# Performance work log

Hardware: AMD Instinct MI355X
Metric: run time of the kernel (lower is better)

The kernel has to match this reference:

```python
import jax, jax.numpy as jnp
import numpy as np

N_NODES = 100000
N_EDGES = 1600000
N_EMBED = 48
N_CONVS = 6
N_GRAPHS = 1000
VOCAB = 100


def setup_inputs() -> dict:
    key = jax.random.key(0)
    ks = jax.random.split(key, 20)
    AtomicNum = jax.random.randint(ks[0], (N_NODES,), 0, VOCAB)
    Edge = jax.random.randint(ks[1], (2, N_EDGES), 0, N_NODES)
    graph_id = jnp.sort(jax.random.randint(ks[2], (N_NODES,), 0, N_GRAPHS))
    s = 1.0 / np.sqrt(N_EMBED)
    def lin(k):
        k1, k2 = jax.random.split(k)
        w = jax.random.uniform(k1, (N_EMBED, N_EMBED), jnp.float32, -s, s)
        b = jax.random.uniform(k2, (N_EMBED,), jnp.float32, -s, s)
        return w, b
    def stacked(k):
        ws, bs = zip(*[lin(kk) for kk in jax.random.split(k, N_CONVS)])
        return jnp.stack(ws), jnp.stack(bs)
    emb = jax.random.normal(ks[3], (VOCAB, N_EMBED), jnp.float32)
    msg_w1, msg_b1 = stacked(ks[4])
    msg_w2, msg_b2 = stacked(ks[5])
    upd_w1, upd_b1 = stacked(ks[6])
    upd_w2, upd_b2 = stacked(ks[7])
    ro_w1, ro_b1 = lin(ks[8])
    k1, k2 = jax.random.split(ks[9])
    ro_w2 = jax.random.uniform(k1, (N_EMBED, 1), jnp.float32, -s, s)
    ro_b2 = jax.random.uniform(k2, (1,), jnp.float32, -s, s)
    return dict(AtomicNum=AtomicNum, Edge=Edge, graph_id=graph_id, emb=emb,
                msg_w1=msg_w1, msg_b1=msg_b1, msg_w2=msg_w2, msg_b2=msg_b2,
                upd_w1=upd_w1, upd_b1=upd_b1, upd_w2=upd_w2, upd_b2=upd_b2,
                ro_w1=ro_w1, ro_b1=ro_b1, ro_w2=ro_w2, ro_b2=ro_b2)


def reference(AtomicNum, Edge, graph_id, emb,
              msg_w1, msg_b1, msg_w2, msg_b2,
              upd_w1, upd_b1, upd_w2, upd_b2,
              ro_w1, ro_b1, ro_w2, ro_b2):
    n_nodes = AtomicNum.shape[0]
    src, dst = Edge[0], Edge[1]
    h = emb[AtomicNum]  # [N, d]
    for l in range(N_CONVS):
        # gather endpoint features, elementwise product, message MLP
        x = h[src] * h[dst]                                      # [E, d]
        m = jax.nn.relu(x @ msg_w1[l] + msg_b1[l]) @ msg_w2[l] + msg_b2[l]
        agg = jax.ops.segment_sum(m, dst, num_segments=n_nodes)  # scatter_add
        u = jax.nn.relu(agg @ upd_w1[l] + upd_b1[l]) @ upd_w2[l] + upd_b2[l]
        h = h + u  # residual update
    y = jax.nn.relu(h @ ro_w1 + ro_b1) @ ro_w2 + ro_b2           # [N, 1]
    # per-graph sum readout (== torch.split by Natom + sum per chunk)
    out = jax.ops.segment_sum(y[:, 0], graph_id, num_segments=N_GRAPHS)
    return out
```

## Files before the change

kernel.cpp:

```cpp
#include <hip/hip_runtime.h>
#include <hip/hip_bf16.h>


#define NE 48
#define NB_SH 8

typedef __attribute__((ext_vector_type(8))) short short8;
typedef __attribute__((ext_vector_type(4))) float floatx4;

__device__ __forceinline__ unsigned short bf16_rne(float v) {
    unsigned u = __float_as_uint(v);
    u += 0x7FFFu + ((u >> 16) & 1u);
    return (unsigned short)(u >> 16);
}

__device__ __forceinline__ void split8p(const float* __restrict__ x, short8& hi, short8& lo) {
    union { unsigned u[4]; short8 s; } H, L;
#pragma unroll
    for (int i = 0; i < 4; ++i) {
        float a = x[2 * i], b = x[2 * i + 1];
        __hip_bfloat162 h2 = __float22bfloat162_rn(make_float2(a, b));
        unsigned h = *reinterpret_cast<unsigned*>(&h2);
        float ra = a - __uint_as_float(h << 16);
        float rb = b - __uint_as_float(h & 0xFFFF0000u);
        __hip_bfloat162 l2 = __float22bfloat162_rn(make_float2(ra, rb));
        H.u[i] = h;
        L.u[i] = *reinterpret_cast<unsigned*>(&l2);
    }
    hi = H.s; lo = L.s;
}

__device__ __forceinline__ void gemm3(const short8& ah0, const short8& al0,
                                      const short8& ah1, const short8& al1,
                                      const short8* __restrict__ hi,
                                      const short8* __restrict__ lo,
                                      int lane, floatx4* acc) {
#pragma unroll
    for (int t = 0; t < 3; ++t) {
        short8 bh0 = hi[(t * 2 + 0) * 64 + lane];
        short8 bh1 = hi[(t * 2 + 1) * 64 + lane];
        short8 bl0 = lo[(t * 2 + 0) * 64 + lane];
        short8 bl1 = lo[(t * 2 + 1) * 64 + lane];
        floatx4 c = {0.0f, 0.0f, 0.0f, 0.0f};
        c = __builtin_amdgcn_mfma_f32_16x16x32_bf16(ah0, bh0, c, 0, 0, 0);
        c = __builtin_amdgcn_mfma_f32_16x16x32_bf16(ah1, bh1, c, 0, 0, 0);
        c = __builtin_amdgcn_mfma_f32_16x16x32_bf16(al0, bh0, c, 0, 0, 0);
        c = __builtin_amdgcn_mfma_f32_16x16x32_bf16(al1, bh1, c, 0, 0, 0);
        c = __builtin_amdgcn_mfma_f32_16x16x32_bf16(ah0, bl0, c, 0, 0, 0);
        c = __builtin_amdgcn_mfma_f32_16x16x32_bf16(ah1, bl1, c, 0, 0, 0);
        acc[t] = c;
    }
}

__global__ __launch_bounds__(256) void embed_kernel(const int* __restrict__ an,
                                                    const float* __restrict__ emb,
                                                    float* __restrict__ h, int n4) {
    int i = blockIdx.x * 256 + threadIdx.x;
    if (i >= n4) return;
    int n = i / 12, q = i - n * 12;
    ((float4*)h)[i] = ((const float4*)emb)[an[n] * 12 + q];
}

__global__ __launch_bounds__(256) void hist_kernel(const int* __restrict__ dst,
                                                   int* __restrict__ cnt, int E) {
    int e = blockIdx.x * 256 + threadIdx.x;
    if (e < E) atomicAdd(&cnt[dst[e]], 1);
}

__global__ __launch_bounds__(256) void scansum_kernel(const int* __restrict__ cnt,
                                                      int* __restrict__ bsum, int N) {
    __shared__ int sw[4];
    const int tid = threadIdx.x, lane = tid & 63, wid = tid >> 6;
    int base = blockIdx.x * 1024;
    int v = 0;
#pragma unroll
    for (int k = 0; k < 4; ++k) {
        int i = base + k * 256 + tid;
        v += (i < N) ? cnt[i] : 0;
    }
#pragma unroll
    for (int o = 1; o < 64; o <<= 1) v += __shfl_xor(v, o, 64);
    if (lane == 0) sw[wid] = v;
    __syncthreads();
    if (tid == 0) bsum[blockIdx.x] = sw[0] + sw[1] + sw[2] + sw[3];
}

__global__ __launch_bounds__(256) void scanb_kernel(int* __restrict__ bsum, int nblk) {
    __shared__ int s[256];
    int tid = threadIdx.x;
    s[tid] = (tid < nblk) ? bsum[tid] : 0;
    __syncthreads();
    if (tid == 0) {
        int run = 0;
        for (int i = 0; i < nblk; ++i) { int t = s[i]; s[i] = run; run += t; }
    }
    __syncthreads();
    if (tid < nblk) bsum[tid] = s[tid];
}

__global__ __launch_bounds__(1024) void scanfix_kernel(const int* __restrict__ cnt,
                                                       const int* __restrict__ bsum,
                                                       int* __restrict__ offs,
                                                       int* __restrict__ gpos, int N) {
    __shared__ int swave[16];
    const int tid = threadIdx.x, lane = tid & 63, wid = tid >> 6;
    int i = blockIdx.x * 1024 + tid;
    int orig = (i < N) ? cnt[i] : 0;
    int v = orig;
#pragma unroll
    for (int off = 1; off < 64; off <<= 1) {
        int u = __shfl_up(v, off, 64);
        if (lane >= off) v += u;
    }
    if (lane == 63) swave[wid] = v;
    __syncthreads();
    if (wid == 0) {
        int w = (lane < 16) ? swave[lane] : 0;
#pragma unroll
        for (int off = 1; off < 16; off <<= 1) {
            int u = __shfl_up(w, off, 64);
            if (lane >= off) w += u;
        }
        if (lane < 16) swave[lane] = w;
    }
    __syncthreads();
    int prefix = (wid > 0) ? swave[wid - 1] : 0;
    int val = bsum[blockIdx.x] + prefix + v - orig;
    if (i < N) {
        offs[i] = val;
        if ((i & 255) == 0) gpos[i >> 8] = val;
    }
}

__global__ __launch_bounds__(256) void partA_kernel(const int* __restrict__ src,
                                                    const int* __restrict__ dst,
                                                    int* __restrict__ gpos,
                                                    int2* __restrict__ pairbuf,
                                                    int E, int NB) {
    __shared__ int lhist[512];
    __shared__ int lbase[512];
    const int tid = threadIdx.x;
    for (int i = tid; i < NB; i += 256) lhist[i] = 0;
    __syncthreads();
    const int base = blockIdx.x * 2048;
    int ssrc[8], sdst[8], rnk[8];
#pragma unroll
    for (int k = 0; k < 8; ++k) {
        int e = base + k * 256 + tid;
        if (e < E) {
            ssrc[k] = src[e]; sdst[k] = dst[e];
            rnk[k] = atomicAdd(&lhist[sdst[k] >> NB_SH], 1);
        }
    }
    __syncthreads();
    for (int i = tid; i < NB; i += 256) {
        int c = lhist[i];
        lbase[i] = c ? atomicAdd(&gpos[i], c) : 0;
    }
    __syncthreads();
#pragma unroll
    for (int k = 0; k < 8; ++k) {
        int e = base + k * 256 + tid;
        if (e < E)
            pairbuf[lbase[sdst[k] >> NB_SH] + rnk[k]] = make_int2(ssrc[k], sdst[k]);
    }
}

__global__ __launch_bounds__(256) void partB_kernel(const int2* __restrict__ pairbuf,
                                                    int* __restrict__ offs,
                                                    int* __restrict__ colsrc, int E) {
    int e = blockIdx.x * 256 + threadIdx.x;
    if (e < E) {
        int2 p = pairbuf[e];
        int pos = atomicAdd(&offs[p.y], 1);
        colsrc[pos] = p.x;
    }
}

__global__ __launch_bounds__(256) void pack_all_kernel(const float* __restrict__ w0,
                                                       const float* __restrict__ w1m,
                                                       const float* __restrict__ w2m,
                                                       const float* __restrict__ w3m,
                                                       const float* __restrict__ w4m,
                                                       short8* __restrict__ hi,
                                                       short8* __restrict__ lo) {
    int idx = blockIdx.x * 256 + threadIdx.x;
    if (idx >= 4 * 2304 + 384) return;
    int slot = idx / 2304;
    int rem  = idx - slot * 2304;
    const float* w = (slot == 0) ? w0 : (slot == 1) ? w1m : (slot == 2) ? w2m
                   : (slot == 3) ? w3m : w4m;
    int lane = rem & 63;
    int s = (rem >> 6) & 1;
    int t = (rem >> 7) % 3;
    int l = (rem >> 7) / 3;
    short8 h8, l8;
#pragma unroll
    for (int i = 0; i < 8; ++i) {
        int k = s * 32 + (lane >> 4) * 8 + i;
        int j = t * 16 + (lane & 15);
        float v = (k < NE) ? w[l * NE * NE + k * NE + j] : 0.0f;
        unsigned short hh = bf16_rne(v);
        float hf = __uint_as_float((unsigned)hh << 16);
        unsigned short ll = bf16_rne(v - hf);
        h8[i] = (short)hh;
        l8[i] = (short)ll;
    }
    hi[idx] = h8;
    lo[idx] = l8;
}

__global__ __launch_bounds__(256, 2) void layer_kernel(
    const float* __restrict__ hin,
    const int* __restrict__ colsrc,
    const int* __restrict__ ends,
    const int* __restrict__ cnt,
    float* __restrict__ hout,
    const short8* __restrict__ bhi,
    const short8* __restrict__ blo,
    const float* __restrict__ b1,
    const short8* __restrict__ w2hi, const short8* __restrict__ w2lo, const float* __restrict__ b2,
    const short8* __restrict__ u1hi, const short8* __restrict__ u1lo, const float* __restrict__ ub1,
    const short8* __restrict__ u2hi, const short8* __restrict__ u2lo, const float* __restrict__ ub2,
    int N,
    int final_layer,
    const int* __restrict__ gid,
    const short8* __restrict__ rw1hi, const short8* __restrict__ rw1lo,
    const float* __restrict__ rb1, const float* __restrict__ rw2,
    const float* __restrict__ rb2, float* __restrict__ out)
{
    __shared__ float tile[4][16][52];
    const int tid  = threadIdx.x;
    const int lane = tid & 63;
    const int wid  = tid >> 6;
    const int n0   = blockIdx.x * 64 + wid * 16;
    if (n0 >= N) return;

    const int m  = lane & 15;
    const int kb = lane >> 4;
    float (*mytile)[52] = tile[wid];

    short8 bh[6], bl[6];
#pragma unroll
    for (int i = 0; i < 6; ++i) { bh[i] = bhi[i * 64 + lane]; bl[i] = blo[i * 64 + lane]; }
    const float bb0 = b1[m], bb1 = b1[16 + m], bb2 = b1[32 + m];

#pragma unroll 1
    for (int nn = 0; nn < 16; ++nn) {
        const int n = n0 + nn;
        const int deg = cnt[n];
        const int end = ends[n];
        const int beg = end - deg;

        const float* hd = hin + (size_t)n * NE;
        float4 d0a = ((const float4*)(hd + kb * 8))[0];
        float4 d0b = ((const float4*)(hd + kb * 8))[1];
        float4 d1a = make_float4(0, 0, 0, 0), d1b = d1a;
        if (kb < 2) {
            d1a = ((const float4*)(hd + 32 + kb * 8))[0];
            d1b = ((const float4*)(hd + 32 + kb * 8))[1];
        }

        float s0 = 0.0f, s1 = 0.0f, s2 = 0.0f;
        const int ntile = (deg + 15) >> 4;

        for (int it = 0; it < ntile; ++it) {
            const int rem = deg - it * 16;
            int eidx = beg + it * 16 + m;
            int srow = colsrc[(m < rem) ? eidx : beg];
            const float* hs = hin + (size_t)srow * NE + kb * 8;

            float x0[8], x1[8];
            {
                float4 a0 = ((const float4*)hs)[0];
                float4 a1 = ((const float4*)hs)[1];
                x0[0] = a0.x * d0a.x; x0[1] = a0.y * d0a.y; x0[2] = a0.z * d0a.z; x0[3] = a0.w * d0a.w;
                x0[4] = a1.x * d0b.x; x0[5] = a1.y * d0b.y; x0[6] = a1.z * d0b.z; x0[7] = a1.w * d0b.w;
            }
            if (kb < 2) {
                float4 a0 = ((const float4*)(hs + 32))[0];
                float4 a1 = ((const float4*)(hs + 32))[1];
                x1[0] = a0.x * d1a.x; x1[1] = a0.y * d1a.y; x1[2] = a0.z * d1a.z; x1[3] = a0.w * d1a.w;
                x1[4] = a1.x * d1b.x; x1[5] = a1.y * d1b.y; x1[6] = a1.z * d1b.z; x1[7] = a1.w * d1b.w;
            } else {
#pragma unroll
                for (int i = 0; i < 8; ++i) x1[i] = 0.0f;
            }

            short8 ah0, al0, ah1, al1;
            split8p(x0, ah0, al0);
            split8p(x1, ah1, al1);

#pragma unroll
            for (int t = 0; t < 3; ++t) {
                short8 bh0 = bh[t * 2 + 0], bh1 = bh[t * 2 + 1];
                short8 bl0 = bl[t * 2 + 0], bl1 = bl[t * 2 + 1];
                floatx4 c = {0.0f, 0.0f, 0.0f, 0.0f};
                c = __builtin_amdgcn_mfma_f32_16x16x32_bf16(ah0, bh0, c, 0, 0, 0);
                c = __builtin_amdgcn_mfma_f32_16x16x32_bf16(ah1, bh1, c, 0, 0, 0);
                c = __builtin_amdgcn_mfma_f32_16x16x32_bf16(al0, bh0, c, 0, 0, 0);
                c = __builtin_amdgcn_mfma_f32_16x16x32_bf16(al1, bh1, c, 0, 0, 0);
                c = __builtin_amdgcn_mfma_f32_16x16x32_bf16(ah0, bl0, c, 0, 0, 0);
                c = __builtin_amdgcn_mfma_f32_16x16x32_bf16(ah1, bl1, c, 0, 0, 0);
                const float bb = (t == 0) ? bb0 : (t == 1) ? bb1 : bb2;
                float ts = 0.0f;
#pragma unroll
                for (int r = 0; r < 4; ++r) {
                    float v = fmaxf(c[r] + bb, 0.0f);
                    v = (kb * 4 + r < rem) ? v : 0.0f;
                    ts += v;
                }
                if (t == 0) s0 += ts; else if (t == 1) s1 += ts; else s2 += ts;
            }
        }

        s0 += __shfl_xor(s0, 16, 64); s0 += __shfl_xor(s0, 32, 64);
        s1 += __shfl_xor(s1, 16, 64); s1 += __shfl_xor(s1, 32, 64);
        s2 += __shfl_xor(s2, 16, 64); s2 += __shfl_xor(s2, 32, 64);

        float t1v = __shfl(s1, lane & 15, 64);
        float t2v = __shfl(s2, lane & 15, 64);
        float val = (lane < 16) ? s0 : (lane < 32) ? t1v : t2v;
        if (lane < 48) mytile[nn][lane] = val;
    }
    asm volatile("s_waitcnt lgkmcnt(0)" ::: "memory");

    float c0[8], c1[8];
    {
        const float* row = &mytile[m][0];
        *(float4*)(c0)     = *(const float4*)(row + kb * 8);
        *(float4*)(c0 + 4) = *(const float4*)(row + kb * 8 + 4);
        if (kb < 2) {
            *(float4*)(c1)     = *(const float4*)(row + 32 + kb * 8);
            *(float4*)(c1 + 4) = *(const float4*)(row + 32 + kb * 8 + 4);
        } else {
#pragma unroll
            for (int i = 0; i < 8; ++i) c1[i] = 0.0f;
        }
    }
    asm volatile("s_waitcnt lgkmcnt(0)" ::: "memory");
    short8 ah0, al0, ah1, al1;
    split8p(c0, ah0, al0);
    split8p(c1, ah1, al1);

    floatx4 acc[3];
    gemm3(ah0, al0, ah1, al1, w2hi, w2lo, lane, acc);

    {
        float b2j[3];
#pragma unroll
        for (int t = 0; t < 3; ++t) b2j[t] = b2[t * 16 + m];
#pragma unroll
        for (int r = 0; r < 4; ++r) {
            float fd = (float)cnt[n0 + kb * 4 + r];
#pragma unroll
            for (int t = 0; t < 3; ++t) acc[t][r] = fmaf(fd, b2j[t], acc[t][r]);
        }
    }

#pragma unroll
    for (int t = 0; t < 3; ++t)
#pragma unroll
        for (int r = 0; r < 4; ++r)
            mytile[kb * 4 + r][t * 16 + m] = acc[t][r];
    asm volatile("s_waitcnt lgkmcnt(0)" ::: "memory");
    {
        const float* row = &mytile[m][0];
        *(float4*)(c0)     = *(const float4*)(row + kb * 8);
        *(float4*)(c0 + 4) = *(const float4*)(row + kb * 8 + 4);
        if (kb < 2) {
            *(float4*)(c1)     = *(const float4*)(row + 32 + kb * 8);
            *(float4*)(c1 + 4) = *(const float4*)(row + 32 + kb * 8 + 4);
        } else {
#pragma unroll
            for (int i = 0; i < 8; ++i) c1[i] = 0.0f;
        }
    }
    asm volatile("s_waitcnt lgkmcnt(0)" ::: "memory");
    split8p(c0, ah0, al0);
    split8p(c1, ah1, al1);
    gemm3(ah0, al0, ah1, al1, u1hi, u1lo, lane, acc);
    {
        float bj[3];
#pragma unroll
        for (int t = 0; t < 3; ++t) bj[t] = ub1[t * 16 + m];
#pragma unroll
        for (int t = 0; t < 3; ++t)
#pragma unroll
            for (int r = 0; r < 4; ++r)
                acc[t][r] = fmaxf(acc[t][r] + bj[t], 0.0f);
    }

#pragma unroll
    for (int t = 0; t < 3; ++t)
#pragma unroll
        for (int r = 0; r < 4; ++r)
            mytile[kb * 4 + r][t * 16 + m] = acc[t][r];
    asm volatile("s_waitcnt lgkmcnt(0)" ::: "memory");
    {
        const float* row = &mytile[m][0];
        *(float4*)(c0)     = *(const float4*)(row + kb * 8);
        *(float4*)(c0 + 4) = *(const float4*)(row + kb * 8 + 4);
        if (kb < 2) {
            *(float4*)(c1)     = *(const float4*)(row + 32 + kb * 8);
            *(float4*)(c1 + 4) = *(const float4*)(row + 32 + kb * 8 + 4);
        } else {
#pragma unroll
            for (int i = 0; i < 8; ++i) c1[i] = 0.0f;
        }
    }
    asm volatile("s_waitcnt lgkmcnt(0)" ::: "memory");
    split8p(c0, ah0, al0);
    split8p(c1, ah1, al1);
    gemm3(ah0, al0, ah1, al1, u2hi, u2lo, lane, acc);

    {
        float bj[3];
#pragma unroll
        for (int t = 0; t < 3; ++t) bj[t] = ub2[t * 16 + m];
#pragma unroll
        for (int r = 0; r < 4; ++r) {
            const size_t row = (size_t)(n0 + kb * 4 + r) * NE;
#pragma unroll
            for (int t = 0; t < 3; ++t)
                acc[t][r] += hin[row + t * 16 + m] + bj[t];
        }
    }

    if (!final_layer) {
#pragma unroll
        for (int r = 0; r < 4; ++r) {
            const size_t row = (size_t)(n0 + kb * 4 + r) * NE;
#pragma unroll
            for (int t = 0; t < 3; ++t)
                hout[row + t * 16 + m] = acc[t][r];
        }
        return;
    }

#pragma unroll
    for (int t = 0; t < 3; ++t)
#pragma unroll
        for (int r = 0; r < 4; ++r)
            mytile[kb * 4 + r][t * 16 + m] = acc[t][r];
    asm volatile("s_waitcnt lgkmcnt(0)" ::: "memory");
    {
        const float* row = &mytile[m][0];
        *(float4*)(c0)     = *(const float4*)(row + kb * 8);
        *(float4*)(c0 + 4) = *(const float4*)(row + kb * 8 + 4);
        if (kb < 2) {
            *(float4*)(c1)     = *(const float4*)(row + 32 + kb * 8);
            *(float4*)(c1 + 4) = *(const float4*)(row + 32 + kb * 8 + 4);
        } else {
#pragma unroll
            for (int i = 0; i < 8; ++i) c1[i] = 0.0f;
        }
    }
    split8p(c0, ah0, al0);
    split8p(c1, ah1, al1);
    gemm3(ah0, al0, ah1, al1, rw1hi, rw1lo, lane, acc);

    float p[4] = {0.0f, 0.0f, 0.0f, 0.0f};
    {
        float bj[3], wj[3];
#pragma unroll
        for (int t = 0; t < 3; ++t) { bj[t] = rb1[t * 16 + m]; wj[t] = rw2[t * 16 + m]; }
#pragma unroll
        for (int t = 0; t < 3; ++t)
#pragma unroll
            for (int r = 0; r < 4; ++r)
                p[r] = fmaf(fmaxf(acc[t][r] + bj[t], 0.0f), wj[t], p[r]);
    }
#pragma unroll
    for (int o = 1; o < 16; o <<= 1) {
#pragma unroll
        for (int r = 0; r < 4; ++r) p[r] += __shfl_xor(p[r], o, 16);
    }
    if (m == 0) {
        float b2v = rb2[0];
#pragma unroll
        for (int r = 0; r < 4; ++r) {
            int n = n0 + kb * 4 + r;
            atomicAdd(out + gid[n], p[r] + b2v);
        }
    }
}

extern "C" void kernel_launch(void* const* d_in, const int* in_sizes, int n_in,
                              void* d_out, int out_size, void* d_ws, size_t ws_size,
                              hipStream_t stream) {
    const int*   AtomicNum = (const int*)  d_in[0];
    const int*   Edge      = (const int*)  d_in[1];
    const int*   graph_id  = (const int*)  d_in[2];
    const float* emb       = (const float*)d_in[3];
    const float* msg_w1    = (const float*)d_in[4];
    const float* msg_b1    = (const float*)d_in[5];
    const float* msg_w2    = (const float*)d_in[6];
    const float* msg_b2    = (const float*)d_in[7];
    const float* upd_w1    = (const float*)d_in[8];
    const float* upd_b1    = (const float*)d_in[9];
    const float* upd_w2    = (const float*)d_in[10];
    const float* upd_b2    = (const float*)d_in[11];
    const float* ro_w1     = (const float*)d_in[12];
    const float* ro_b1     = (const float*)d_in[13];
    const float* ro_w2     = (const float*)d_in[14];
    const float* ro_b2     = (const float*)d_in[15];

    const int N = in_sizes[0];
    const int E = in_sizes[1] / 2;
    const int* src = Edge;
    const int* dst = Edge + E;
    const int NB = (N + 255) >> NB_SH;
    const int NBLK = (N + 1023) / 1024;

    float*  h    = (float*)d_ws;
    float*  h2   = h  + (size_t)N * NE;
    int*    cnt  = (int*)(h2 + (size_t)N * NE);
    int*    offs = cnt + N;
    int*    colsrc = offs + N;
    short8* whi  = (short8*)(colsrc + E);
    short8* wlo  = whi + (4 * 2304 + 384);
    int*    gpos = (int*)(wlo + (4 * 2304 + 384));
    int*    bsum = gpos + NB;
    int2*   pairbuf = (int2*)h2;

    hipMemsetAsync(d_out, 0, (size_t)out_size * sizeof(float), stream);
    hipMemsetAsync(cnt, 0, (size_t)N * sizeof(int), stream);

    int n4 = N * 12;
    embed_kernel<<<(n4 + 255) / 256, 256, 0, stream>>>(AtomicNum, emb, h, n4);

    hist_kernel<<<(E + 255) / 256, 256, 0, stream>>>(dst, cnt, E);
    scansum_kernel<<<NBLK, 256, 0, stream>>>(cnt, bsum, N);
    scanb_kernel<<<1, 256, 0, stream>>>(bsum, NBLK);
    scanfix_kernel<<<NBLK, 1024, 0, stream>>>(cnt, bsum, offs, gpos, N);
    partA_kernel<<<(E + 2047) / 2048, 256, 0, stream>>>(src, dst, gpos, pairbuf, E, NB);
    partB_kernel<<<(E + 255) / 256, 256, 0, stream>>>(pairbuf, offs, colsrc, E);

    pack_all_kernel<<<(4 * 2304 + 384 + 255) / 256, 256, 0, stream>>>(
        msg_w1, msg_w2, upd_w1, upd_w2, ro_w1, whi, wlo);

    const float* hin = h;
    float* hout = h2;
    for (int l = 0; l < 6; ++l) {
        layer_kernel<<<(N + 63) / 64, 256, 0, stream>>>(
            hin, colsrc, offs, cnt, hout,
            whi + 0 * 2304 + (size_t)l * 384, wlo + 0 * 2304 + (size_t)l * 384,
            msg_b1 + (size_t)l * NE,
            whi + 1 * 2304 + (size_t)l * 384, wlo + 1 * 2304 + (size_t)l * 384, msg_b2 + (size_t)l * NE,
            whi + 2 * 2304 + (size_t)l * 384, wlo + 2 * 2304 + (size_t)l * 384, upd_b1 + (size_t)l * NE,
            whi + 3 * 2304 + (size_t)l * 384, wlo + 3 * 2304 + (size_t)l * 384, upd_b2 + (size_t)l * NE,
            N,
            (l == 5) ? 1 : 0,
            graph_id,
            whi + 4 * 2304, wlo + 4 * 2304,
            ro_b1, ro_w2, ro_b2, (float*)d_out);
        const float* tmp = hin; hin = hout; hout = (float*)tmp;
    }
}
```

Baseline: 870.0 us.

## Software-pipeline edge gathers across nodes with flattened tile cursor and LDS-staged dst rows

Replaces the per-node nested edge loop with a flattened cursor over all 16-edge tiles of the wave's 16 nodes. The colsrc index load runs two tiles ahead and the source-row gather one tile ahead, using double-buffered registers, so gather latency overlaps with the MFMA compute and does not stall at node boundaries. The wave's 16 destination rows are staged in LDS once and reused for the products and the residual add. Degrees are loaded once per lane and broadcast with shuffles. This costs extra registers and LDS, which could reduce occupancy, and adds branchy cursor logic.

```diff
diff --git a/kernel.cpp b/kernel.cpp
--- a/kernel.cpp
+++ b/kernel.cpp
@@ -209,6 +209,8 @@
     hi[idx] = h8;
     lo[idx] = l8;
 }
+
+struct Cur { int nn; int e0; int rem; };
 
 __global__ __launch_bounds__(256, 2) void layer_kernel(
     const float* __restrict__ hin,
@@ -230,6 +232,7 @@
     const float* __restrict__ rb2, float* __restrict__ out)
 {
     __shared__ float tile[4][16][52];
+    __shared__ float hdls[4][16][48];
     const int tid  = threadIdx.x;
     const int lane = tid & 63;
     const int wid  = tid >> 6;
@@ -239,89 +242,149 @@
     const int m  = lane & 15;
     const int kb = lane >> 4;
     float (*mytile)[52] = tile[wid];
+    float (*myhd)[48]   = hdls[wid];
+
+    {
+        const float4* sp = (const float4*)(hin + (size_t)n0 * NE);
+        float4* dp = (float4*)myhd;
+#pragma unroll
+        for (int f = 0; f < 3; ++f) dp[lane + f * 64] = sp[lane + f * 64];
+    }
+    const int mydeg = cnt[n0 + m];
+    const int myend = ends[n0 + m];
 
     short8 bh[6], bl[6];
 #pragma unroll
     for (int i = 0; i < 6; ++i) { bh[i] = bhi[i * 64 + lane]; bl[i] = blo[i * 64 + lane]; }
     const float bb0 = b1[m], bb1 = b1[16 + m], bb2 = b1[32 + m];
 
-#pragma unroll 1
-    for (int nn = 0; nn < 16; ++nn) {
-        const int n = n0 + nn;
-        const int deg = cnt[n];
-        const int end = ends[n];
-        const int beg = end - deg;
-
-        const float* hd = hin + (size_t)n * NE;
-        float4 d0a = ((const float4*)(hd + kb * 8))[0];
-        float4 d0b = ((const float4*)(hd + kb * 8))[1];
-        float4 d1a = make_float4(0, 0, 0, 0), d1b = d1a;
-        if (kb < 2) {
-            d1a = ((const float4*)(hd + 32 + kb * 8))[0];
-            d1b = ((const float4*)(hd + 32 + kb * 8))[1];
-        }
-
-        float s0 = 0.0f, s1 = 0.0f, s2 = 0.0f;
-        const int ntile = (deg + 15) >> 4;
-
-        for (int it = 0; it < ntile; ++it) {
-            const int rem = deg - it * 16;
-            int eidx = beg + it * 16 + m;
-            int srow = colsrc[(m < rem) ? eidx : beg];
-            const float* hs = hin + (size_t)srow * NE + kb * 8;
-
-            float x0[8], x1[8];
-            {
-                float4 a0 = ((const float4*)hs)[0];
-                float4 a1 = ((const float4*)hs)[1];
-                x0[0] = a0.x * d0a.x; x0[1] = a0.y * d0a.y; x0[2] = a0.z * d0a.z; x0[3] = a0.w * d0a.w;
-                x0[4] = a1.x * d0b.x; x0[5] = a1.y * d0b.y; x0[6] = a1.z * d0b.z; x0[7] = a1.w * d0b.w;
-            }
-            if (kb < 2) {
-                float4 a0 = ((const float4*)(hs + 32))[0];
-                float4 a1 = ((const float4*)(hs + 32))[1];
-                x1[0] = a0.x * d1a.x; x1[1] = a0.y * d1a.y; x1[2] = a0.z * d1a.z; x1[3] = a0.w * d1a.w;
-                x1[4] = a1.x * d1b.x; x1[5] = a1.y * d1b.y; x1[6] = a1.z * d1b.z; x1[7] = a1.w * d1b.w;
-            } else {
-#pragma unroll
-                for (int i = 0; i < 8; ++i) x1[i] = 0.0f;
-            }
-
-            short8 ah0, al0, ah1, al1;
-            split8p(x0, ah0, al0);
-            split8p(x1, ah1, al1);
-
-#pragma unroll
-            for (int t = 0; t < 3; ++t) {
-                short8 bh0 = bh[t * 2 + 0], bh1 = bh[t * 2 + 1];
-                short8 bl0 = bl[t * 2 + 0], bl1 = bl[t * 2 + 1];
-                floatx4 c = {0.0f, 0.0f, 0.0f, 0.0f};
-                c = __builtin_amdgcn_mfma_f32_16x16x32_bf16(ah0, bh0, c, 0, 0, 0);
-                c = __builtin_amdgcn_mfma_f32_16x16x32_bf16(ah1, bh1, c, 0, 0, 0);
-                c = __builtin_amdgcn_mfma_f32_16x16x32_bf16(al0, bh0, c, 0, 0, 0);
-                c = __builtin_amdgcn_mfma_f32_16x16x32_bf16(al1, bh1, c, 0, 0, 0);
-                c = __builtin_amdgcn_mfma_f32_16x16x32_bf16(ah0, bl0, c, 0, 0, 0);
-                c = __builtin_amdgcn_mfma_f32_16x16x32_bf16(ah1, bl1, c, 0, 0, 0);
-                const float bb = (t == 0) ? bb0 : (t == 1) ? bb1 : bb2;
-                float ts = 0.0f;
-#pragma unroll
-                for (int r = 0; r < 4; ++r) {
-                    float v = fmaxf(c[r] + bb, 0.0f);
-                    v = (kb * 4 + r < rem) ? v : 0.0f;
-                    ts += v;
-                }
-                if (t == 0) s0 += ts; else if (t == 1) s1 += ts; else s2 += ts;
-            }
-        }
-
+    {
+        float4 z = make_float4(0, 0, 0, 0);
+        float4* zp = (float4*)&mytile[lane >> 2][(lane & 3) * 12];
+        zp[0] = z; zp[1] = z; zp[2] = z;
+    }
+    asm volatile("s_waitcnt lgkmcnt(0)" ::: "memory");
+
+    auto nextc = [&](Cur c) -> Cur {
+        c.e0 += 16; c.rem -= 16;
+        while (c.rem <= 0) {
+            ++c.nn;
+            if (c.nn >= 16) { c.nn = 16; c.e0 = 0; c.rem = 1; return c; }
+            int d = __shfl(mydeg, c.nn, 64);
+            int e = __shfl(myend, c.nn, 64);
+            c.e0 = e - d; c.rem = d;
+        }
+        return c;
+    };
+    auto load_idx = [&](const Cur& c) -> int {
+        int off = (m < c.rem) ? m : 0;
+        return colsrc[c.e0 + off];
+    };
+
+    int curnode = -1;
+    float s0 = 0.0f, s1 = 0.0f, s2 = 0.0f;
+    float4 d0a = make_float4(0,0,0,0), d0b = d0a, d1a = d0a, d1b = d0a;
+
+    auto finalize = [&](int nn) {
         s0 += __shfl_xor(s0, 16, 64); s0 += __shfl_xor(s0, 32, 64);
         s1 += __shfl_xor(s1, 16, 64); s1 += __shfl_xor(s1, 32, 64);
         s2 += __shfl_xor(s2, 16, 64); s2 += __shfl_xor(s2, 32, 64);
-
         float t1v = __shfl(s1, lane & 15, 64);
         float t2v = __shfl(s2, lane & 15, 64);
         float val = (lane < 16) ? s0 : (lane < 32) ? t1v : t2v;
         if (lane < 48) mytile[nn][lane] = val;
+    };
+
+    auto load_hs = [&](int srow, float4& r0, float4& r1, float4& r2, float4& r3) {
+        const float* hs = hin + (size_t)srow * NE + kb * 8;
+        r0 = ((const float4*)hs)[0];
+        r1 = ((const float4*)hs)[1];
+        if (kb < 2) {
+            r2 = ((const float4*)(hs + 32))[0];
+            r3 = ((const float4*)(hs + 32))[1];
+        }
+    };
+
+    auto do_compute = [&](const Cur& c, const float4& r0, const float4& r1,
+                          const float4& r2, const float4& r3) {
+        if (c.nn != curnode) {
+            if (curnode >= 0) finalize(curnode);
+            curnode = c.nn;
+            s0 = s1 = s2 = 0.0f;
+            const float* hr = myhd[c.nn];
+            d0a = ((const float4*)(hr + kb * 8))[0];
+            d0b = ((const float4*)(hr + kb * 8))[1];
+            if (kb < 2) {
+                d1a = ((const float4*)(hr + 32 + kb * 8))[0];
+                d1b = ((const float4*)(hr + 32 + kb * 8))[1];
+            }
+        }
+        float x0[8], x1[8];
+        x0[0] = r0.x * d0a.x; x0[1] = r0.y * d0a.y; x0[2] = r0.z * d0a.z; x0[3] = r0.w * d0a.w;
+        x0[4] = r1.x * d0b.x; x0[5] = r1.y * d0b.y; x0[6] = r1.z * d0b.z; x0[7] = r1.w * d0b.w;
+        if (kb < 2) {
+            x1[0] = r2.x * d1a.x; x1[1] = r2.y * d1a.y; x1[2] = r2.z * d1a.z; x1[3] = r2.w * d1a.w;
+            x1[4] = r3.x * d1b.x; x1[5] = r3.y * d1b.y; x1[6] = r3.z * d1b.z; x1[7] = r3.w * d1b.w;
+        } else {
+#pragma unroll
+            for (int i = 0; i < 8; ++i) x1[i] = 0.0f;
+        }
+        short8 ah0, al0, ah1, al1;
+        split8p(x0, ah0, al0);
+        split8p(x1, ah1, al1);
+#pragma unroll
+        for (int t = 0; t < 3; ++t) {
+            short8 bh0 = bh[t * 2 + 0], bh1 = bh[t * 2 + 1];
+            short8 bl0 = bl[t * 2 + 0], bl1 = bl[t * 2 + 1];
+            floatx4 cc = {0.0f, 0.0f, 0.0f, 0.0f};
+            cc = __builtin_amdgcn_mfma_f32_16x16x32_bf16(ah0, bh0, cc, 0, 0, 0);
+            cc = __builtin_amdgcn_mfma_f32_16x16x32_bf16(ah1, bh1, cc, 0, 0, 0);
+            cc = __builtin_amdgcn_mfma_f32_16x16x32_bf16(al0, bh0, cc, 0, 0, 0);
+            cc = __builtin_amdgcn_mfma_f32_16x16x32_bf16(al1, bh1, cc, 0, 0, 0);
+            cc = __builtin_amdgcn_mfma_f32_16x16x32_bf16(ah0, bl0, cc, 0, 0, 0);
+            cc = __builtin_amdgcn_mfma_f32_16x16x32_bf16(ah1, bl1, cc, 0, 0, 0);
+            const float bb = (t == 0) ? bb0 : (t == 1) ? bb1 : bb2;
+            float ts = 0.0f;
+#pragma unroll
+            for (int r = 0; r < 4; ++r) {
+                float v = fmaxf(cc[r] + bb, 0.0f);
+                v = (kb * 4 + r < c.rem) ? v : 0.0f;
+                ts += v;
+            }
+            if (t == 0) s0 += ts; else if (t == 1) s1 += ts; else s2 += ts;
+        }
+    };
+
+    {
+        Cur cX; cX.nn = -1; cX.e0 = -16; cX.rem = 16;
+        cX = nextc(cX);
+        if (cX.nn < 16) {
+            int idxX = load_idx(cX);
+            Cur cY = nextc(cX);
+            int idxY = (cY.nn < 16) ? load_idx(cY) : 0;
+            float4 A0, A1, A2, A3, B0, B1, B2, B3;
+            A0 = A1 = A2 = A3 = make_float4(0, 0, 0, 0);
+            B0 = B1 = B2 = B3 = A0;
+            load_hs(idxX, A0, A1, A2, A3);
+            Cur cZ = nextc(cY);
+            for (;;) {
+                {
+                    int idxZ = (cZ.nn < 16) ? load_idx(cZ) : 0;
+                    if (cY.nn < 16) load_hs(idxY, B0, B1, B2, B3);
+                    do_compute(cX, A0, A1, A2, A3);
+                    cX = cY; cY = cZ; cZ = nextc(cZ); idxY = idxZ;
+                }
+                if (cX.nn >= 16) break;
+                {
+                    int idxZ = (cZ.nn < 16) ? load_idx(cZ) : 0;
+                    if (cY.nn < 16) load_hs(idxY, A0, A1, A2, A3);
+                    do_compute(cX, B0, B1, B2, B3);
+                    cX = cY; cY = cZ; cZ = nextc(cZ); idxY = idxZ;
+                }
+                if (cX.nn >= 16) break;
+            }
+        }
+        if (curnode >= 0) finalize(curnode);
     }
     asm volatile("s_waitcnt lgkmcnt(0)" ::: "memory");
 
@@ -352,7 +415,7 @@
         for (int t = 0; t < 3; ++t) b2j[t] = b2[t * 16 + m];
 #pragma unroll
         for (int r = 0; r < 4; ++r) {
-            float fd = (float)cnt[n0 + kb * 4 + r];
+            float fd = (float)__shfl(mydeg, kb * 4 + r, 64);
 #pragma unroll
             for (int t = 0; t < 3; ++t) acc[t][r] = fmaf(fd, b2j[t], acc[t][r]);
         }
@@ -420,10 +483,9 @@
         for (int t = 0; t < 3; ++t) bj[t] = ub2[t * 16 + m];
 #pragma unroll
         for (int r = 0; r < 4; ++r) {
-            const size_t row = (size_t)(n0 + kb * 4 + r) * NE;
 #pragma unroll
             for (int t = 0; t < 3; ++t)
-                acc[t][r] += hin[row + t * 16 + m] + bj[t];
+                acc[t][r] += myhd[kb * 4 + r][t * 16 + m] + bj[t];
         }
     }
 
```

New measurement: 861.0 us. No clear change (-1.0%).

## Shrink layer blocks, preload degrees via shuffles, use zero pad row for tails

Applied to the files above, without the earlier changes.

The layer kernel now launches 128-thread blocks covering 32 nodes instead of 256 threads covering 64. Degrees and end offsets for a wave's 16 nodes are loaded once and broadcast with shuffles, rather than reloaded from global memory for every node. Padded edge lanes now point at an extra all-zero row appended to each h buffer, so the per-element validity mask is dropped. The relu(bias) contribution of the padded rows is subtracted analytically afterwards. This trims memory loads and ALU work in the inner loop, at the cost of two extra small memsets and a changed workspace layout.

```diff
diff --git a/kernel.cpp b/kernel.cpp
--- a/kernel.cpp
+++ b/kernel.cpp
@@ -210,7 +210,7 @@
     lo[idx] = l8;
 }
 
-__global__ __launch_bounds__(256, 2) void layer_kernel(
+__global__ __launch_bounds__(128, 4) void layer_kernel(
     const float* __restrict__ hin,
     const int* __restrict__ colsrc,
     const int* __restrict__ ends,
@@ -229,27 +229,32 @@
     const float* __restrict__ rb1, const float* __restrict__ rw2,
     const float* __restrict__ rb2, float* __restrict__ out)
 {
-    __shared__ float tile[4][16][52];
+    __shared__ float tile[2][16][52];
     const int tid  = threadIdx.x;
     const int lane = tid & 63;
     const int wid  = tid >> 6;
-    const int n0   = blockIdx.x * 64 + wid * 16;
+    const int n0   = blockIdx.x * 32 + wid * 16;
     if (n0 >= N) return;
 
     const int m  = lane & 15;
     const int kb = lane >> 4;
     float (*mytile)[52] = tile[wid];
 
+    const int mydeg = cnt[n0 + m];
+    const int myend = ends[n0 + m];
+
     short8 bh[6], bl[6];
 #pragma unroll
     for (int i = 0; i < 6; ++i) { bh[i] = bhi[i * 64 + lane]; bl[i] = blo[i * 64 + lane]; }
     const float bb0 = b1[m], bb1 = b1[16 + m], bb2 = b1[32 + m];
+    const float rbb0 = fmaxf(bb0, 0.0f), rbb1 = fmaxf(bb1, 0.0f), rbb2 = fmaxf(bb2, 0.0f);
+    const float rbb_mine = (lane < 16) ? rbb0 : (lane < 32) ? rbb1 : rbb2;
 
 #pragma unroll 1
     for (int nn = 0; nn < 16; ++nn) {
         const int n = n0 + nn;
-        const int deg = cnt[n];
-        const int end = ends[n];
+        const int deg = __shfl(mydeg, nn, 64);
+        const int end = __shfl(myend, nn, 64);
         const int beg = end - deg;
 
         const float* hd = hin + (size_t)n * NE;
@@ -266,8 +271,7 @@
 
         for (int it = 0; it < ntile; ++it) {
             const int rem = deg - it * 16;
-            int eidx = beg + it * 16 + m;
-            int srow = colsrc[(m < rem) ? eidx : beg];
+            int srow = (m < rem) ? colsrc[beg + it * 16 + m] : N;
             const float* hs = hin + (size_t)srow * NE + kb * 8;
 
             float x0[8], x1[8];
@@ -295,21 +299,18 @@
             for (int t = 0; t < 3; ++t) {
                 short8 bh0 = bh[t * 2 + 0], bh1 = bh[t * 2 + 1];
                 short8 bl0 = bl[t * 2 + 0], bl1 = bl[t * 2 + 1];
-                floatx4 c = {0.0f, 0.0f, 0.0f, 0.0f};
-                c = __builtin_amdgcn_mfma_f32_16x16x32_bf16(ah0, bh0, c, 0, 0, 0);
-                c = __builtin_amdgcn_mfma_f32_16x16x32_bf16(ah1, bh1, c, 0, 0, 0);
-                c = __builtin_amdgcn_mfma_f32_16x16x32_bf16(al0, bh0, c, 0, 0, 0);
-                c = __builtin_amdgcn_mfma_f32_16x16x32_bf16(al1, bh1, c, 0, 0, 0);
-                c = __builtin_amdgcn_mfma_f32_16x16x32_bf16(ah0, bl0, c, 0, 0, 0);
-                c = __builtin_amdgcn_mfma_f32_16x16x32_bf16(ah1, bl1, c, 0, 0, 0);
+                floatx4 cc = {0.0f, 0.0f, 0.0f, 0.0f};
+                cc = __builtin_amdgcn_mfma_f32_16x16x32_bf16(ah0, bh0, cc, 0, 0, 0);
+                cc = __builtin_amdgcn_mfma_f32_16x16x32_bf16(ah1, bh1, cc, 0, 0, 0);
+                cc = __builtin_amdgcn_mfma_f32_16x16x32_bf16(al0, bh0, cc, 0, 0, 0);
+                cc = __builtin_amdgcn_mfma_f32_16x16x32_bf16(al1, bh1, cc, 0, 0, 0);
+                cc = __builtin_amdgcn_mfma_f32_16x16x32_bf16(ah0, bl0, cc, 0, 0, 0);
+                cc = __builtin_amdgcn_mfma_f32_16x16x32_bf16(ah1, bl1, cc, 0, 0, 0);
                 const float bb = (t == 0) ? bb0 : (t == 1) ? bb1 : bb2;
                 float ts = 0.0f;
 #pragma unroll
-                for (int r = 0; r < 4; ++r) {
-                    float v = fmaxf(c[r] + bb, 0.0f);
-                    v = (kb * 4 + r < rem) ? v : 0.0f;
-                    ts += v;
-                }
+                for (int r = 0; r < 4; ++r)
+                    ts += fmaxf(cc[r] + bb, 0.0f);
                 if (t == 0) s0 += ts; else if (t == 1) s1 += ts; else s2 += ts;
             }
         }
@@ -321,6 +322,8 @@
         float t1v = __shfl(s1, lane & 15, 64);
         float t2v = __shfl(s2, lane & 15, 64);
         float val = (lane < 16) ? s0 : (lane < 32) ? t1v : t2v;
+        const float npad = (float)(ntile * 16 - deg);
+        val = fmaf(-npad, rbb_mine, val);
         if (lane < 48) mytile[nn][lane] = val;
     }
     asm volatile("s_waitcnt lgkmcnt(0)" ::: "memory");
@@ -352,7 +355,7 @@
         for (int t = 0; t < 3; ++t) b2j[t] = b2[t * 16 + m];
 #pragma unroll
         for (int r = 0; r < 4; ++r) {
-            float fd = (float)cnt[n0 + kb * 4 + r];
+            float fd = (float)__shfl(mydeg, kb * 4 + r, 64);
 #pragma unroll
             for (int t = 0; t < 3; ++t) acc[t][r] = fmaf(fd, b2j[t], acc[t][r]);
         }
@@ -514,8 +517,8 @@
     const int NBLK = (N + 1023) / 1024;
 
     float*  h    = (float*)d_ws;
-    float*  h2   = h  + (size_t)N * NE;
-    int*    cnt  = (int*)(h2 + (size_t)N * NE);
+    float*  h2   = h  + (size_t)(N + 1) * NE;
+    int*    cnt  = (int*)(h2 + (size_t)(N + 1) * NE);
     int*    offs = cnt + N;
     int*    colsrc = offs + N;
     short8* whi  = (short8*)(colsrc + E);
@@ -526,6 +529,8 @@
 
     hipMemsetAsync(d_out, 0, (size_t)out_size * sizeof(float), stream);
     hipMemsetAsync(cnt, 0, (size_t)N * sizeof(int), stream);
+    hipMemsetAsync(h  + (size_t)N * NE, 0, NE * sizeof(float), stream);
+    hipMemsetAsync(h2 + (size_t)N * NE, 0, NE * sizeof(float), stream);
 
     int n4 = N * 12;
     embed_kernel<<<(n4 + 255) / 256, 256, 0, stream>>>(AtomicNum, emb, h, n4);
@@ -543,7 +548,7 @@
     const float* hin = h;
     float* hout = h2;
     for (int l = 0; l < 6; ++l) {
-        layer_kernel<<<(N + 63) / 64, 256, 0, stream>>>(
+        layer_kernel<<<(N + 31) / 32, 128, 0, stream>>>(
             hin, colsrc, offs, cnt, hout,
             whi + 0 * 2304 + (size_t)l * 384, wlo + 0 * 2304 + (size_t)l * 384,
             msg_b1 + (size_t)l * NE,
```

Result: faster. 832.2 us (-4.3%).
